# Kernel optimization log

Measured on AMD Instinct MI355X. Metric: run time of the kernel, lower is better.

The kernel has to match this reference:

```python
import jax, jax.numpy as jnp
import numpy as np

N = 100000      # nodes
E = 1600000     # edges (before self loops)
F_IN = 256      # num_features
HID = 8         # hid per head, layer 1
H1 = 8          # in_head
H2 = 4          # out_head
NCLS = 40       # num_classes


def setup_inputs() -> dict:
    key = jax.random.key(0)
    ks = jax.random.split(key, 10)
    p = lambda k, shape: jax.random.normal(k, shape, jnp.float32) * 0.1
    d1 = H1 * HID   # 64
    d2 = H2 * NCLS  # 160
    return dict(
        x=jax.random.normal(ks[0], (N, F_IN), jnp.float32),
        edge_index=jax.random.randint(ks[1], (2, E), 0, N),
        Wl1=p(ks[2], (F_IN, d1)), bl1=jnp.zeros((d1,), jnp.float32),
        Wr1=p(ks[3], (F_IN, d1)), br1=jnp.zeros((d1,), jnp.float32),
        att1=p(ks[4], (H1, HID)), b1=jnp.zeros((d1,), jnp.float32),
        Wl2=p(ks[5], (d1, d2)), bl2=jnp.zeros((d2,), jnp.float32),
        Wr2=p(ks[6], (d1, d2)), br2=jnp.zeros((d2,), jnp.float32),
        att2=p(ks[7], (H2, NCLS)), b2=jnp.zeros((NCLS,), jnp.float32),
    )


def gatv2_conv(x, src, dst, Wl, bl, Wr, br, att, bias, heads, ch, concat):
    """PyG GATv2Conv (eval mode): lin_l -> source/messages, lin_r -> target."""
    n = x.shape[0]
    xl = (x @ Wl + bl).reshape(n, heads, ch)   # source-side features
    xr = (x @ Wr + br).reshape(n, heads, ch)   # target-side features
    # edge-wise attention logits: LeakyReLU(x_i + x_j) . att
    e = jax.nn.leaky_relu(xl[src] + xr[dst], 0.2)          # [E, H, C]
    logits = jnp.einsum('ehc,hc->eh', e, att)               # [E, H]
    # segment softmax over incoming edges of each destination node
    m = jax.ops.segment_max(logits, dst, num_segments=n)    # [N, H]
    ex = jnp.exp(logits - m[dst])
    s = jax.ops.segment_sum(ex, dst, num_segments=n)        # [N, H]
    alpha = ex / (s[dst] + 1e-16)                           # [E, H]
    # scatter-add weighted source messages
    out = jax.ops.segment_sum(xl[src] * alpha[:, :, None], dst, num_segments=n)  # [N, H, C]
    if concat:
        return out.reshape(n, heads * ch) + bias
    return out.mean(axis=1) + bias


def reference(x, edge_index, Wl1, bl1, Wr1, br1, att1, b1,
              Wl2, bl2, Wr2, br2, att2, b2):
    n = x.shape[0]
    loop = jnp.arange(n)
    # PyG GATv2Conv default add_self_loops=True
    src = jnp.concatenate([edge_index[0], loop])
    dst = jnp.concatenate([edge_index[1], loop])
    # eval mode: all dropout (input, inter-layer, attention) disabled
    h = gatv2_conv(x, src, dst, Wl1, bl1, Wr1, br1, att1, b1, H1, HID, True)
    h = jax.nn.elu(h)
    out = gatv2_conv(h, src, dst, Wl2, bl2, Wr2, br2, att2, b2, H2, NCLS, False)
    return jax.nn.log_softmax(out, axis=1)
```

## Files before the change

### kernel.cpp

```cpp
#include <hip/hip_runtime.h>
#include <math.h>

#define NN 100000
#define EE 1600000
#define FIN 256
#define D1 64
#define D2 160
#define C2 40
#define PK1 264
#define PK2 72
#define NBUCK 391
#define CAP 5000

typedef unsigned short u16;
typedef __attribute__((ext_vector_type(8))) short bf16x8;
typedef __attribute__((ext_vector_type(4))) float f32x4;

__device__ __forceinline__ float bf2f(u16 u){ return __uint_as_float((unsigned)u << 16); }
__device__ __forceinline__ u16 f2bf(float f){
  unsigned b = __float_as_uint(f);
  return (u16)((b + 0x7FFFu + ((b >> 16) & 1u)) >> 16);
}

__global__ void wprep_k(const float* __restrict__ Wl1, const float* __restrict__ Wr1,
                        const float* __restrict__ att1,
                        const float* __restrict__ bl1, const float* __restrict__ br1,
                        const float* __restrict__ Wl2, const float* __restrict__ Wr2,
                        const float* __restrict__ att2,
                        const float* __restrict__ bl2, const float* __restrict__ br2,
                        float* __restrict__ WA1, float* __restrict__ BA1,
                        float* __restrict__ WA2, float* __restrict__ BA2){
  int t = threadIdx.x;
  {
    int k = t;
    #pragma unroll
    for (int j = 0; j < 16; ++j){
      const float* W = (j < 8) ? Wl1 : Wr1;
      int h = j & 7;
      float s = 0.f;
      #pragma unroll
      for (int c = 0; c < 8; ++c) s += W[(size_t)k*D1 + h*8 + c] * att1[h*8 + c];
      WA1[k*16 + j] = 0.6f * s;
    }
  }
  if (t < 64){
    int k = t;
    #pragma unroll
    for (int j = 0; j < 8; ++j){
      const float* W = (j < 4) ? Wl2 : Wr2;
      int h = j & 3;
      float s = 0.f;
      for (int c = 0; c < 40; ++c) s += W[(size_t)k*D2 + h*40 + c] * att2[h*40 + c];
      WA2[k*8 + j] = 0.6f * s;
    }
  }
  if (t >= 128 && t < 144){
    int j = t - 128;
    const float* B = (j < 8) ? bl1 : br1;
    int h = j & 7;
    float s = 0.f;
    #pragma unroll
    for (int c = 0; c < 8; ++c) s += B[h*8 + c] * att1[h*8 + c];
    BA1[j] = 0.6f * s;
  }
  if (t >= 160 && t < 168){
    int j = t - 160;
    const float* B = (j < 4) ? bl2 : br2;
    int h = j & 3;
    float s = 0.f;
    for (int c = 0; c < 40; ++c) s += B[h*40 + c] * att2[h*40 + c];
    BA2[j] = 0.6f * s;
  }
}

__global__ __launch_bounds__(256) void part1_k(const int* __restrict__ ei,
                                               int* __restrict__ bcnt,
                                               int* __restrict__ csrtmp){
  __shared__ int hist[NBUCK];
  __shared__ int gbase[NBUCK];
  int t = threadIdx.x;
  for (int i = t; i < NBUCK; i += 256) hist[i] = 0;
  __syncthreads();
  int rb[8], rr[8], rv[8];
  #pragma unroll
  for (int q = 0; q < 8; ++q){
    int e = blockIdx.x*2048 + q*256 + t;
    rb[q] = -1;
    if (e < EE){
      int s = ei[e], d = ei[EE + e];
      int b = d >> 8;
      rb[q] = b;
      rv[q] = s | ((d & 255) << 17);
      rr[q] = atomicAdd(&hist[b], 1);
    }
  }
  __syncthreads();
  for (int i = t; i < NBUCK; i += 256)
    if (hist[i] > 0) gbase[i] = atomicAdd(&bcnt[i], hist[i]);
  __syncthreads();
  #pragma unroll
  for (int q = 0; q < 8; ++q){
    if (rb[q] >= 0){
      int pos = gbase[rb[q]] + rr[q];
      if (pos < CAP) csrtmp[rb[q]*CAP + pos] = rv[q];
    }
  }
}

__global__ __launch_bounds__(256) void sort_k(const int* __restrict__ bcnt,
                                              const int* __restrict__ csrtmp,
                                              int* __restrict__ csr,
                                              int* __restrict__ off,
                                              int* __restrict__ end){
  __shared__ int cnt[256];
  __shared__ int sc[256];
  __shared__ int cur[256];
  int b = blockIdx.x, t = threadIdx.x;
  int E = bcnt[b]; if (E > CAP) E = CAP;
  cnt[t] = 0;
  __syncthreads();
  for (int i = t; i < E; i += 256){
    int v = csrtmp[b*CAP + i];
    atomicAdd(&cnt[(v >> 17) & 255], 1);
  }
  __syncthreads();
  int x = cnt[t];
  sc[t] = x;
  __syncthreads();
  for (int o = 1; o < 256; o <<= 1){
    int v = (t >= o) ? sc[t - o] : 0;
    __syncthreads();
    sc[t] += v;
    __syncthreads();
  }
  int excl = sc[t] - x;
  cur[t] = excl;
  int n = (b << 8) + t;
  if (n < NN){
    off[n] = b*CAP + excl;
    end[n] = b*CAP + excl + x;
  }
  __syncthreads();
  for (int i = t; i < E; i += 256){
    int v = csrtmp[b*CAP + i];
    int p = atomicAdd(&cur[(v >> 17) & 255], 1);
    csr[b*CAP + p] = v & 0x1FFFF;
  }
}

__global__ __launch_bounds__(256) void gemm1_mfma(
    const float* __restrict__ X,
    const float* __restrict__ Wl, const float* __restrict__ bl,
    const float* __restrict__ Wr, const float* __restrict__ br,
    const float* __restrict__ WA1, const float* __restrict__ BA1,
    u16* __restrict__ outl, u16* __restrict__ outr, float* __restrict__ ALR){
  __shared__ u16 WB[144*PK1];
  int t = threadIdx.x;
  #pragma unroll
  for (int q = 0; q < 16; ++q){
    int idx = t + 256*q;
    int k = idx >> 4, c4 = idx & 15;
    float4 vl = *reinterpret_cast<const float4*>(Wl + (size_t)k*D1 + c4*4);
    float4 vr = *reinterpret_cast<const float4*>(Wr + (size_t)k*D1 + c4*4);
    WB[(c4*4+0)*PK1 + k] = f2bf(vl.x); WB[(c4*4+1)*PK1 + k] = f2bf(vl.y);
    WB[(c4*4+2)*PK1 + k] = f2bf(vl.z); WB[(c4*4+3)*PK1 + k] = f2bf(vl.w);
    WB[(64+c4*4+0)*PK1 + k] = f2bf(vr.x); WB[(64+c4*4+1)*PK1 + k] = f2bf(vr.y);
    WB[(64+c4*4+2)*PK1 + k] = f2bf(vr.z); WB[(64+c4*4+3)*PK1 + k] = f2bf(vr.w);
  }
  #pragma unroll
  for (int q = 0; q < 16; ++q){
    int idx = t + 256*q;
    int k = idx >> 4, j = idx & 15;
    WB[(128+j)*PK1 + k] = f2bf(WA1[k*16 + j]);
  }
  __syncthreads();
  int w = t >> 6, l = t & 63;
  int g = l >> 4;
  int arow = blockIdx.x*64 + w*16 + (l & 15);
  if (arow >= NN) arow = NN-1;
  const float* xp = X + (size_t)arow*FIN + g*8;
  f32x4 acc[9] = {};
  #pragma unroll
  for (int kk = 0; kk < 8; ++kk){
    float4 a0 = *reinterpret_cast<const float4*>(xp + kk*32);
    float4 a1 = *reinterpret_cast<const float4*>(xp + kk*32 + 4);
    union { bf16x8 v; u16 u[8]; } A;
    A.u[0]=f2bf(a0.x); A.u[1]=f2bf(a0.y); A.u[2]=f2bf(a0.z); A.u[3]=f2bf(a0.w);
    A.u[4]=f2bf(a1.x); A.u[5]=f2bf(a1.y); A.u[6]=f2bf(a1.z); A.u[7]=f2bf(a1.w);
    const u16* wb = WB + (l & 15)*PK1 + kk*32 + g*8;
    #pragma unroll
    for (int c = 0; c < 9; ++c){
      bf16x8 B = *reinterpret_cast<const bf16x8*>(wb + c*16*PK1);
      acc[c] = __builtin_amdgcn_mfma_f32_16x16x32_bf16(A.v, B, acc[c], 0, 0, 0);
    }
  }
  int ocol = l & 15;
  int orow0 = blockIdx.x*64 + w*16 + g*4;
  #pragma unroll
  for (int c = 0; c < 8; ++c){
    bool left = (c < 4);
    int col = (left ? c : c-4)*16 + ocol;
    u16* op = left ? outl : outr;
    float bv = (left ? bl : br)[col];
    #pragma unroll
    for (int r = 0; r < 4; ++r){
      int row = orow0 + r;
      if (row < NN) op[(size_t)row*D1 + col] = f2bf(acc[c][r] + bv);
    }
  }
  {
    float bav = BA1[ocol];
    #pragma unroll
    for (int r = 0; r < 4; ++r){
      int row = orow0 + r;
      if (row < NN) ALR[(size_t)row*16 + ocol] = acc[8][r] + bav;
    }
  }
}

__global__ __launch_bounds__(256) void gemm2_mfma(
    const u16* __restrict__ H,
    const float* __restrict__ Wl, const float* __restrict__ bl,
    const float* __restrict__ Wr, const float* __restrict__ br,
    const float* __restrict__ WA2, const float* __restrict__ BA2,
    u16* __restrict__ outl, u16* __restrict__ outr, float* __restrict__ ALR){
  __shared__ u16 WB[336*PK2];
  int t = threadIdx.x;
  #pragma unroll
  for (int q = 0; q < 10; ++q){
    int idx = t + 256*q;
    int k = idx / 40, c4 = idx % 40;
    float4 vl = *reinterpret_cast<const float4*>(Wl + (size_t)k*D2 + c4*4);
    float4 vr = *reinterpret_cast<const float4*>(Wr + (size_t)k*D2 + c4*4);
    WB[(c4*4+0)*PK2 + k] = f2bf(vl.x); WB[(c4*4+1)*PK2 + k] = f2bf(vl.y);
    WB[(c4*4+2)*PK2 + k] = f2bf(vl.z); WB[(c4*4+3)*PK2 + k] = f2bf(vl.w);
    WB[(160+c4*4+0)*PK2 + k] = f2bf(vr.x); WB[(160+c4*4+1)*PK2 + k] = f2bf(vr.y);
    WB[(160+c4*4+2)*PK2 + k] = f2bf(vr.z); WB[(160+c4*4+3)*PK2 + k] = f2bf(vr.w);
  }
  #pragma unroll
  for (int q = 0; q < 2; ++q){
    int i2 = t + 256*q;
    int k = i2 >> 3, j = i2 & 7;
    WB[(320+j)*PK2 + k] = f2bf(WA2[k*8 + j]);
    WB[(328+j)*PK2 + k] = 0;
  }
  __syncthreads();
  int w = t >> 6, l = t & 63;
  int g = l >> 4;
  int arow = blockIdx.x*64 + w*16 + (l & 15);
  if (arow >= NN) arow = NN-1;
  const u16* hp = H + (size_t)arow*D1 + g*8;
  f32x4 acc[21] = {};
  #pragma unroll
  for (int kk = 0; kk < 2; ++kk){
    bf16x8 A = *reinterpret_cast<const bf16x8*>(hp + kk*32);
    const u16* wb = WB + (l & 15)*PK2 + kk*32 + g*8;
    #pragma unroll
    for (int c = 0; c < 21; ++c){
      bf16x8 B = *reinterpret_cast<const bf16x8*>(wb + c*16*PK2);
      acc[c] = __builtin_amdgcn_mfma_f32_16x16x32_bf16(A, B, acc[c], 0, 0, 0);
    }
  }
  int ocol = l & 15;
  int orow0 = blockIdx.x*64 + w*16 + g*4;
  #pragma unroll
  for (int c = 0; c < 20; ++c){
    bool left = (c < 10);
    int col = (left ? c : c-10)*16 + ocol;
    u16* op = left ? outl : outr;
    float bv = (left ? bl : br)[col];
    #pragma unroll
    for (int r = 0; r < 4; ++r){
      int row = orow0 + r;
      if (row < NN) op[(size_t)row*D2 + col] = f2bf(acc[c][r] + bv);
    }
  }
  if (ocol < 8){
    float bav = BA2[ocol];
    #pragma unroll
    for (int r = 0; r < 4; ++r){
      int row = orow0 + r;
      if (row < NN) ALR[(size_t)row*8 + ocol] = acc[20][r] + bav;
    }
  }
}

__global__ void l1_fused(const u16* __restrict__ xl, const u16* __restrict__ xr,
                         const int* __restrict__ off, const int* __restrict__ end,
                         const int* __restrict__ csr,
                         const float* __restrict__ att, const float* __restrict__ ALR,
                         const float* __restrict__ b, u16* __restrict__ out){
  int tid = threadIdx.x;
  int lane = tid & 63;
  int nh = lane >> 5, g = (lane >> 4) & 1, l = lane & 15;
  int n = blockIdx.x*8 + (tid >> 6)*2 + nh;
  if (n >= NN) return;
  int h = l >> 1;
  ushort4 xru = *reinterpret_cast<const ushort4*>(xr + (size_t)n*D1 + 4*l);
  float xrv[4] = {bf2f(xru.x), bf2f(xru.y), bf2f(xru.z), bf2f(xru.w)};
  float a04[4];
  #pragma unroll
  for (int k = 0; k < 4; ++k) a04[k] = 0.4f * att[4*l + k];
  float ARn = ALR[(size_t)n*16 + 8 + h];
  ushort4 xsu = *reinterpret_cast<const ushort4*>(xl + (size_t)n*D1 + 4*l);
  float xsv[4] = {bf2f(xsu.x), bf2f(xsu.y), bf2f(xsu.z), bf2f(xsu.w)};
  float ts = 0.f;
  #pragma unroll
  for (int k = 0; k < 4; ++k) ts += a04[k] * fabsf(xsv[k] + xrv[k]);
  ts += __shfl_xor(ts, 1);
  float ps = (g == 0) ? __expf(ts + ALR[(size_t)n*16 + h] + ARn) : 0.f;
  float s = ps, acc[4];
  #pragma unroll
  for (int k = 0; k < 4; ++k) acc[k] = ps * xsv[k];
  int p = off[n] + g, e1 = end[n];
  for (; p + 2 < e1; p += 4){
    int sa = csr[p], sb = csr[p+2];
    ushort4 ua = *reinterpret_cast<const ushort4*>(xl + (size_t)sa*D1 + 4*l);
    ushort4 ub = *reinterpret_cast<const ushort4*>(xl + (size_t)sb*D1 + 4*l);
    float ALa = ALR[(size_t)sa*16 + h], ALb = ALR[(size_t)sb*16 + h];
    float xa[4] = {bf2f(ua.x), bf2f(ua.y), bf2f(ua.z), bf2f(ua.w)};
    float xb[4] = {bf2f(ub.x), bf2f(ub.y), bf2f(ub.z), bf2f(ub.w)};
    float ta = 0.f, tb = 0.f;
    #pragma unroll
    for (int k = 0; k < 4; ++k){
      ta += a04[k] * fabsf(xa[k] + xrv[k]);
      tb += a04[k] * fabsf(xb[k] + xrv[k]);
    }
    ta += __shfl_xor(ta, 1);
    tb += __shfl_xor(tb, 1);
    float pa = __expf(ta + ALa + ARn);
    float pb = __expf(tb + ALb + ARn);
    s += pa + pb;
    #pragma unroll
    for (int k = 0; k < 4; ++k) acc[k] = fmaf(pa, xa[k], fmaf(pb, xb[k], acc[k]));
  }
  for (; p < e1; p += 2){
    int sa = csr[p];
    ushort4 ua = *reinterpret_cast<const ushort4*>(xl + (size_t)sa*D1 + 4*l);
    float ALa = ALR[(size_t)sa*16 + h];
    float xa[4] = {bf2f(ua.x), bf2f(ua.y), bf2f(ua.z), bf2f(ua.w)};
    float ta = 0.f;
    #pragma unroll
    for (int k = 0; k < 4; ++k) ta += a04[k] * fabsf(xa[k] + xrv[k]);
    ta += __shfl_xor(ta, 1);
    float pa = __expf(ta + ALa + ARn);
    s += pa;
    #pragma unroll
    for (int k = 0; k < 4; ++k) acc[k] = fmaf(pa, xa[k], acc[k]);
  }
  s += __shfl_xor(s, 16);
  #pragma unroll
  for (int k = 0; k < 4; ++k) acc[k] += __shfl_xor(acc[k], 16);
  if (g == 0){
    float inv = 1.f / (s + 1e-16f);
    ushort4 o;
    float v0 = acc[0]*inv + b[4*l+0]; o.x = f2bf(v0 > 0.f ? v0 : expm1f(v0));
    float v1 = acc[1]*inv + b[4*l+1]; o.y = f2bf(v1 > 0.f ? v1 : expm1f(v1));
    float v2 = acc[2]*inv + b[4*l+2]; o.z = f2bf(v2 > 0.f ? v2 : expm1f(v2));
    float v3 = acc[3]*inv + b[4*l+3]; o.w = f2bf(v3 > 0.f ? v3 : expm1f(v3));
    *reinterpret_cast<ushort4*>(out + (size_t)n*D1 + 4*l) = o;
  }
}

__global__ void l2_fused(const u16* __restrict__ xl, const u16* __restrict__ xr,
                         const int* __restrict__ off, const int* __restrict__ end,
                         const int* __restrict__ csr,
                         const float* __restrict__ att, const float* __restrict__ ALR,
                         const float* __restrict__ b, float* __restrict__ out){
  int tid = threadIdx.x;
  int lane = tid & 63;
  int nh = lane >> 5, g = (lane >> 4) & 1, l = lane & 15;
  int n = blockIdx.x*8 + (tid >> 6)*2 + nh;
  if (n >= NN) return;
  int h = l >> 2;
  int c0 = 10*l;
  float xrv[10], a04[10];
  #pragma unroll
  for (int k2 = 0; k2 < 5; ++k2){
    ushort2 u = *reinterpret_cast<const ushort2*>(xr + (size_t)n*D2 + c0 + 2*k2);
    xrv[2*k2] = bf2f(u.x); xrv[2*k2+1] = bf2f(u.y);
  }
  #pragma unroll
  for (int k = 0; k < 10; ++k) a04[k] = 0.4f * att[c0 + k];
  float ARn = ALR[(size_t)n*8 + 4 + h];
  float xsv[10];
  #pragma unroll
  for (int k2 = 0; k2 < 5; ++k2){
    ushort2 u = *reinterpret_cast<const ushort2*>(xl + (size_t)n*D2 + c0 + 2*k2);
    xsv[2*k2] = bf2f(u.x); xsv[2*k2+1] = bf2f(u.y);
  }
  float ts = 0.f;
  #pragma unroll
  for (int k = 0; k < 10; ++k) ts += a04[k] * fabsf(xsv[k] + xrv[k]);
  ts += __shfl_xor(ts, 1); ts += __shfl_xor(ts, 2);
  float ps = (g == 0) ? __expf(ts + ALR[(size_t)n*8 + h] + ARn) : 0.f;
  float s = ps, acc[10];
  #pragma unroll
  for (int k = 0; k < 10; ++k) acc[k] = ps * xsv[k];
  int p = off[n] + g, e1 = end[n];
  for (; p + 2 < e1; p += 4){
    int sa = csr[p], sb = csr[p+2];
    float ALa = ALR[(size_t)sa*8 + h], ALb = ALR[(size_t)sb*8 + h];
    float xa[10], xb[10];
    #pragma unroll
    for (int k2 = 0; k2 < 5; ++k2){
      ushort2 u = *reinterpret_cast<const ushort2*>(xl + (size_t)sa*D2 + c0 + 2*k2);
      xa[2*k2] = bf2f(u.x); xa[2*k2+1] = bf2f(u.y);
    }
    #pragma unroll
    for (int k2 = 0; k2 < 5; ++k2){
      ushort2 u = *reinterpret_cast<const ushort2*>(xl + (size_t)sb*D2 + c0 + 2*k2);
      xb[2*k2] = bf2f(u.x); xb[2*k2+1] = bf2f(u.y);
    }
    float ta = 0.f, tb = 0.f;
    #pragma unroll
    for (int k = 0; k < 10; ++k){
      ta += a04[k] * fabsf(xa[k] + xrv[k]);
      tb += a04[k] * fabsf(xb[k] + xrv[k]);
    }
    ta += __shfl_xor(ta, 1); ta += __shfl_xor(ta, 2);
    tb += __shfl_xor(tb, 1); tb += __shfl_xor(tb, 2);
    float pa = __expf(ta + ALa + ARn);
    float pb = __expf(tb + ALb + ARn);
    s += pa + pb;
    #pragma unroll
    for (int k = 0; k < 10; ++k) acc[k] = fmaf(pa, xa[k], fmaf(pb, xb[k], acc[k]));
  }
  for (; p < e1; p += 2){
    int sa = csr[p];
    float ALa = ALR[(size_t)sa*8 + h];
    float xa[10];
    #pragma unroll
    for (int k2 = 0; k2 < 5; ++k2){
      ushort2 u = *reinterpret_cast<const ushort2*>(xl + (size_t)sa*D2 + c0 + 2*k2);
      xa[2*k2] = bf2f(u.x); xa[2*k2+1] = bf2f(u.y);
    }
    float ta = 0.f;
    #pragma unroll
    for (int k = 0; k < 10; ++k) ta += a04[k] * fabsf(xa[k] + xrv[k]);
    ta += __shfl_xor(ta, 1); ta += __shfl_xor(ta, 2);
    float pa = __expf(ta + ALa + ARn);
    s += pa;
    #pragma unroll
    for (int k = 0; k < 10; ++k) acc[k] = fmaf(pa, xa[k], acc[k]);
  }
  s += __shfl_xor(s, 16);
  #pragma unroll
  for (int k = 0; k < 10; ++k) acc[k] += __shfl_xor(acc[k], 16);
  float inv = 1.f / (s + 1e-16f);
  float v[10];
  #pragma unroll
  for (int k = 0; k < 10; ++k){
    float o = acc[k] * inv;
    o += __shfl_xor(o, 4);
    o += __shfl_xor(o, 8);
    v[k] = o*0.25f + b[10*(l & 3) + k];
  }
  float mx = v[0];
  #pragma unroll
  for (int k = 1; k < 10; ++k) mx = fmaxf(mx, v[k]);
  mx = fmaxf(mx, __shfl_xor(mx, 1));
  mx = fmaxf(mx, __shfl_xor(mx, 2));
  float es = 0.f;
  #pragma unroll
  for (int k = 0; k < 10; ++k) es += __expf(v[k] - mx);
  es += __shfl_xor(es, 1);
  es += __shfl_xor(es, 2);
  float lse = mx + __logf(es);
  if (g == 0 && l < 4){
    float* op = out + (size_t)n*C2 + 10*l;
    #pragma unroll
    for (int k2 = 0; k2 < 5; ++k2)
      *reinterpret_cast<float2*>(op + 2*k2) = make_float2(v[2*k2] - lse, v[2*k2+1] - lse);
  }
}

extern "C" void kernel_launch(void* const* d_in, const int* in_sizes, int n_in,
                              void* d_out, int out_size, void* d_ws, size_t ws_size,
                              hipStream_t stream){
  const float* x    = (const float*)d_in[0];
  const int*   ei   = (const int*)  d_in[1];
  const float* Wl1  = (const float*)d_in[2];
  const float* bl1  = (const float*)d_in[3];
  const float* Wr1  = (const float*)d_in[4];
  const float* br1  = (const float*)d_in[5];
  const float* att1 = (const float*)d_in[6];
  const float* b1   = (const float*)d_in[7];
  const float* Wl2  = (const float*)d_in[8];
  const float* bl2  = (const float*)d_in[9];
  const float* Wr2  = (const float*)d_in[10];
  const float* br2  = (const float*)d_in[11];
  const float* att2 = (const float*)d_in[12];
  const float* b2   = (const float*)d_in[13];
  float* out = (float*)d_out;

  char* ws = (char*)d_ws;
  u16*   B1     = (u16*)  (ws);
  u16*   B2     = (u16*)  (ws + 13000000);
  u16*   h1     = (u16*)  (ws + 26000000);
  u16*   B3     = (u16*)  (ws + 39000000);
  u16*   B4     = (u16*)  (ws + 71000000);
  int*   csrtmp = (int*)  (ws + 71000000);
  float* ALR1   = (float*)(ws + 103000000);
  float* ALR2   = (float*)(ws + 110000000);
  float* WA1    = (float*)(ws + 113300000);
  float* BA1    = (float*)(ws + 113330000);
  float* WA2    = (float*)(ws + 113340000);
  float* BA2    = (float*)(ws + 113350000);
  int*   off    = (int*)  (ws + 113400000);
  int*   end    = (int*)  (ws + 113900000);
  int*   bcnt   = (int*)  (ws + 114400000);
  int*   csr    = (int*)  (ws + 114500000);
  const int blk = 256;
  const int MB = (NN + 63)/64;

  hipMemsetAsync(bcnt, 0, (size_t)NBUCK*4, stream);
  part1_k<<<(EE + 2047)/2048, blk, 0, stream>>>(ei, bcnt, csrtmp);
  sort_k <<<NBUCK, blk, 0, stream>>>(bcnt, csrtmp, csr, off, end);
  wprep_k<<<1, blk, 0, stream>>>(Wl1, Wr1, att1, bl1, br1,
                                 Wl2, Wr2, att2, bl2, br2, WA1, BA1, WA2, BA2);

  gemm1_mfma<<<MB, blk, 0, stream>>>(x, Wl1, bl1, Wr1, br1, WA1, BA1, B1, B2, ALR1);
  l1_fused  <<<(NN + 7)/8, blk, 0, stream>>>(B1, B2, off, end, csr, att1, ALR1, b1, h1);

  gemm2_mfma<<<MB, blk, 0, stream>>>(h1, Wl2, bl2, Wr2, br2, WA2, BA2, B3, B4, ALR2);
  l2_fused  <<<(NN + 7)/8, blk, 0, stream>>>(B3, B4, off, end, csr, att2, ALR2, b2, out);
}
```

Before: 381.3 us.

## Fold target attention term out and store exp source weight inline with features

The target-side linear attention term is constant per destination, so it cancels in the softmax and is dropped. The source-side term is precomputed as exp() in bf16 and stored in padded columns of the source feature rows, replacing a separate fp32 ALR gather per edge. The row strides are padded (72/168) so the per-edge weight arrives with the feature fetch, and wprep is parallelised across 19 blocks. This costs bf16 precision on the exp weight and removes the max-free logit offset, so it risks overflow or loss of accuracy.

```diff
diff --git a/kernel.cpp b/kernel.cpp
--- a/kernel.cpp
+++ b/kernel.cpp
@@ -7,6 +7,8 @@
 #define D1 64
 #define D2 160
 #define C2 40
+#define P1R 72
+#define P2R 168
 #define PK1 264
 #define PK2 72
 #define NBUCK 391
@@ -30,45 +32,39 @@
                         const float* __restrict__ bl2, const float* __restrict__ br2,
                         float* __restrict__ WA1, float* __restrict__ BA1,
                         float* __restrict__ WA2, float* __restrict__ BA2){
-  int t = threadIdx.x;
-  {
-    int k = t;
-    #pragma unroll
-    for (int j = 0; j < 16; ++j){
-      const float* W = (j < 8) ? Wl1 : Wr1;
-      int h = j & 7;
+  int t = blockIdx.x*256 + threadIdx.x;
+  if (t < 4096){
+    int k = t >> 4, j = t & 15;
+    float v = 0.f;
+    if (j < 8){
       float s = 0.f;
       #pragma unroll
-      for (int c = 0; c < 8; ++c) s += W[(size_t)k*D1 + h*8 + c] * att1[h*8 + c];
-      WA1[k*16 + j] = 0.6f * s;
-    }
-  }
-  if (t < 64){
-    int k = t;
-    #pragma unroll
-    for (int j = 0; j < 8; ++j){
-      const float* W = (j < 4) ? Wl2 : Wr2;
-      int h = j & 3;
+      for (int c = 0; c < 8; ++c) s += Wl1[(size_t)k*D1 + j*8 + c] * att1[j*8 + c];
+      v = 0.6f * s;
+    }
+    WA1[t] = v;
+  } else if (t < 4608){
+    int i = t - 4096;
+    int k = i >> 3, j = i & 7;
+    float v = 0.f;
+    if (j < 4){
       float s = 0.f;
-      for (int c = 0; c < 40; ++c) s += W[(size_t)k*D2 + h*40 + c] * att2[h*40 + c];
-      WA2[k*8 + j] = 0.6f * s;
-    }
-  }
-  if (t >= 128 && t < 144){
-    int j = t - 128;
-    const float* B = (j < 8) ? bl1 : br1;
-    int h = j & 7;
+      #pragma unroll
+      for (int c = 0; c < 40; ++c) s += Wl2[(size_t)k*D2 + j*40 + c] * att2[j*40 + c];
+      v = 0.6f * s;
+    }
+    WA2[i] = v;
+  } else if (t < 4616){
+    int j = t - 4608;
     float s = 0.f;
     #pragma unroll
-    for (int c = 0; c < 8; ++c) s += B[h*8 + c] * att1[h*8 + c];
+    for (int c = 0; c < 8; ++c) s += bl1[j*8 + c] * att1[j*8 + c];
     BA1[j] = 0.6f * s;
-  }
-  if (t >= 160 && t < 168){
-    int j = t - 160;
-    const float* B = (j < 4) ? bl2 : br2;
-    int h = j & 3;
+  } else if (t < 4620){
+    int j = t - 4616;
     float s = 0.f;
-    for (int c = 0; c < 40; ++c) s += B[h*40 + c] * att2[h*40 + c];
+    #pragma unroll
+    for (int c = 0; c < 40; ++c) s += bl2[j*40 + c] * att2[j*40 + c];
     BA2[j] = 0.6f * s;
   }
 }
@@ -153,7 +149,7 @@
     const float* __restrict__ Wl, const float* __restrict__ bl,
     const float* __restrict__ Wr, const float* __restrict__ br,
     const float* __restrict__ WA1, const float* __restrict__ BA1,
-    u16* __restrict__ outl, u16* __restrict__ outr, float* __restrict__ ALR){
+    u16* __restrict__ outl, u16* __restrict__ outr){
   __shared__ u16 WB[144*PK1];
   int t = threadIdx.x;
   #pragma unroll
@@ -205,15 +201,15 @@
     #pragma unroll
     for (int r = 0; r < 4; ++r){
       int row = orow0 + r;
-      if (row < NN) op[(size_t)row*D1 + col] = f2bf(acc[c][r] + bv);
-    }
-  }
-  {
+      if (row < NN) op[(size_t)row*P1R + col] = f2bf(acc[c][r] + bv);
+    }
+  }
+  if (ocol < 8){
     float bav = BA1[ocol];
     #pragma unroll
     for (int r = 0; r < 4; ++r){
       int row = orow0 + r;
-      if (row < NN) ALR[(size_t)row*16 + ocol] = acc[8][r] + bav;
+      if (row < NN) outl[(size_t)row*P1R + 64 + ocol] = f2bf(__expf(acc[8][r] + bav));
     }
   }
 }
@@ -223,7 +219,7 @@
     const float* __restrict__ Wl, const float* __restrict__ bl,
     const float* __restrict__ Wr, const float* __restrict__ br,
     const float* __restrict__ WA2, const float* __restrict__ BA2,
-    u16* __restrict__ outl, u16* __restrict__ outr, float* __restrict__ ALR){
+    u16* __restrict__ outl, u16* __restrict__ outr){
   __shared__ u16 WB[336*PK2];
   int t = threadIdx.x;
   #pragma unroll
@@ -272,15 +268,15 @@
     #pragma unroll
     for (int r = 0; r < 4; ++r){
       int row = orow0 + r;
-      if (row < NN) op[(size_t)row*D2 + col] = f2bf(acc[c][r] + bv);
-    }
-  }
-  if (ocol < 8){
+      if (row < NN) op[(size_t)row*P2R + col] = f2bf(acc[c][r] + bv);
+    }
+  }
+  if (ocol < 4){
     float bav = BA2[ocol];
     #pragma unroll
     for (int r = 0; r < 4; ++r){
       int row = orow0 + r;
-      if (row < NN) ALR[(size_t)row*8 + ocol] = acc[20][r] + bav;
+      if (row < NN) outl[(size_t)row*P2R + 160 + ocol] = f2bf(__expf(acc[20][r] + bav));
     }
   }
 }
@@ -288,7 +284,7 @@
 __global__ void l1_fused(const u16* __restrict__ xl, const u16* __restrict__ xr,
                          const int* __restrict__ off, const int* __restrict__ end,
                          const int* __restrict__ csr,
-                         const float* __restrict__ att, const float* __restrict__ ALR,
+                         const float* __restrict__ att,
                          const float* __restrict__ b, u16* __restrict__ out){
   int tid = threadIdx.x;
   int lane = tid & 63;
@@ -296,54 +292,55 @@
   int n = blockIdx.x*8 + (tid >> 6)*2 + nh;
   if (n >= NN) return;
   int h = l >> 1;
-  ushort4 xru = *reinterpret_cast<const ushort4*>(xr + (size_t)n*D1 + 4*l);
+  ushort4 xru = *reinterpret_cast<const ushort4*>(xr + (size_t)n*P1R + 4*l);
   float xrv[4] = {bf2f(xru.x), bf2f(xru.y), bf2f(xru.z), bf2f(xru.w)};
   float a04[4];
   #pragma unroll
   for (int k = 0; k < 4; ++k) a04[k] = 0.4f * att[4*l + k];
-  float ARn = ALR[(size_t)n*16 + 8 + h];
-  ushort4 xsu = *reinterpret_cast<const ushort4*>(xl + (size_t)n*D1 + 4*l);
+  ushort4 xsu = *reinterpret_cast<const ushort4*>(xl + (size_t)n*P1R + 4*l);
+  float wN = bf2f(xl[(size_t)n*P1R + 64 + h]);
   float xsv[4] = {bf2f(xsu.x), bf2f(xsu.y), bf2f(xsu.z), bf2f(xsu.w)};
   float ts = 0.f;
   #pragma unroll
-  for (int k = 0; k < 4; ++k) ts += a04[k] * fabsf(xsv[k] + xrv[k]);
+  for (int k = 0; k < 4; ++k) ts = fmaf(a04[k], fabsf(xsv[k] + xrv[k]), ts);
   ts += __shfl_xor(ts, 1);
-  float ps = (g == 0) ? __expf(ts + ALR[(size_t)n*16 + h] + ARn) : 0.f;
+  float ps = (g == 0) ? __expf(ts) * wN : 0.f;
   float s = ps, acc[4];
   #pragma unroll
   for (int k = 0; k < 4; ++k) acc[k] = ps * xsv[k];
   int p = off[n] + g, e1 = end[n];
   for (; p + 2 < e1; p += 4){
     int sa = csr[p], sb = csr[p+2];
-    ushort4 ua = *reinterpret_cast<const ushort4*>(xl + (size_t)sa*D1 + 4*l);
-    ushort4 ub = *reinterpret_cast<const ushort4*>(xl + (size_t)sb*D1 + 4*l);
-    float ALa = ALR[(size_t)sa*16 + h], ALb = ALR[(size_t)sb*16 + h];
+    ushort4 ua = *reinterpret_cast<const ushort4*>(xl + (size_t)sa*P1R + 4*l);
+    ushort4 ub = *reinterpret_cast<const ushort4*>(xl + (size_t)sb*P1R + 4*l);
+    float wA = bf2f(xl[(size_t)sa*P1R + 64 + h]);
+    float wB = bf2f(xl[(size_t)sb*P1R + 64 + h]);
     float xa[4] = {bf2f(ua.x), bf2f(ua.y), bf2f(ua.z), bf2f(ua.w)};
     float xb[4] = {bf2f(ub.x), bf2f(ub.y), bf2f(ub.z), bf2f(ub.w)};
     float ta = 0.f, tb = 0.f;
     #pragma unroll
     for (int k = 0; k < 4; ++k){
-      ta += a04[k] * fabsf(xa[k] + xrv[k]);
-      tb += a04[k] * fabsf(xb[k] + xrv[k]);
+      ta = fmaf(a04[k], fabsf(xa[k] + xrv[k]), ta);
+      tb = fmaf(a04[k], fabsf(xb[k] + xrv[k]), tb);
     }
     ta += __shfl_xor(ta, 1);
     tb += __shfl_xor(tb, 1);
-    float pa = __expf(ta + ALa + ARn);
-    float pb = __expf(tb + ALb + ARn);
+    float pa = __expf(ta) * wA;
+    float pb = __expf(tb) * wB;
     s += pa + pb;
     #pragma unroll
     for (int k = 0; k < 4; ++k) acc[k] = fmaf(pa, xa[k], fmaf(pb, xb[k], acc[k]));
   }
   for (; p < e1; p += 2){
     int sa = csr[p];
-    ushort4 ua = *reinterpret_cast<const ushort4*>(xl + (size_t)sa*D1 + 4*l);
-    float ALa = ALR[(size_t)sa*16 + h];
+    ushort4 ua = *reinterpret_cast<const ushort4*>(xl + (size_t)sa*P1R + 4*l);
+    float wA = bf2f(xl[(size_t)sa*P1R + 64 + h]);
     float xa[4] = {bf2f(ua.x), bf2f(ua.y), bf2f(ua.z), bf2f(ua.w)};
     float ta = 0.f;
     #pragma unroll
-    for (int k = 0; k < 4; ++k) ta += a04[k] * fabsf(xa[k] + xrv[k]);
+    for (int k = 0; k < 4; ++k) ta = fmaf(a04[k], fabsf(xa[k] + xrv[k]), ta);
     ta += __shfl_xor(ta, 1);
-    float pa = __expf(ta + ALa + ARn);
+    float pa = __expf(ta) * wA;
     s += pa;
     #pragma unroll
     for (int k = 0; k < 4; ++k) acc[k] = fmaf(pa, xa[k], acc[k]);
@@ -365,7 +362,7 @@
 __global__ void l2_fused(const u16* __restrict__ xl, const u16* __restrict__ xr,
                          const int* __restrict__ off, const int* __restrict__ end,
                          const int* __restrict__ csr,
-                         const float* __restrict__ att, const float* __restrict__ ALR,
+                         const float* __restrict__ att,
                          const float* __restrict__ b, float* __restrict__ out){
   int tid = threadIdx.x;
   int lane = tid & 63;
@@ -377,69 +374,76 @@
   float xrv[10], a04[10];
   #pragma unroll
   for (int k2 = 0; k2 < 5; ++k2){
-    ushort2 u = *reinterpret_cast<const ushort2*>(xr + (size_t)n*D2 + c0 + 2*k2);
+    ushort2 u = *reinterpret_cast<const ushort2*>(xr + (size_t)n*P2R + c0 + 2*k2);
     xrv[2*k2] = bf2f(u.x); xrv[2*k2+1] = bf2f(u.y);
   }
   #pragma unroll
   for (int k = 0; k < 10; ++k) a04[k] = 0.4f * att[c0 + k];
-  float ARn = ALR[(size_t)n*8 + 4 + h];
   float xsv[10];
   #pragma unroll
   for (int k2 = 0; k2 < 5; ++k2){
-    ushort2 u = *reinterpret_cast<const ushort2*>(xl + (size_t)n*D2 + c0 + 2*k2);
+    ushort2 u = *reinterpret_cast<const ushort2*>(xl + (size_t)n*P2R + c0 + 2*k2);
     xsv[2*k2] = bf2f(u.x); xsv[2*k2+1] = bf2f(u.y);
   }
+  float wN = bf2f(xl[(size_t)n*P2R + 160 + h]);
   float ts = 0.f;
   #pragma unroll
-  for (int k = 0; k < 10; ++k) ts += a04[k] * fabsf(xsv[k] + xrv[k]);
+  for (int k = 0; k < 10; ++k) ts = fmaf(a04[k], fabsf(xsv[k] + xrv[k]), ts);
   ts += __shfl_xor(ts, 1); ts += __shfl_xor(ts, 2);
-  float ps = (g == 0) ? __expf(ts + ALR[(size_t)n*8 + h] + ARn) : 0.f;
+  float ps = (g == 0) ? __expf(ts) * wN : 0.f;
   float s = ps, acc[10];
   #pragma unroll
   for (int k = 0; k < 10; ++k) acc[k] = ps * xsv[k];
   int p = off[n] + g, e1 = end[n];
   for (; p + 2 < e1; p += 4){
     int sa = csr[p], sb = csr[p+2];
-    float ALa = ALR[(size_t)sa*8 + h], ALb = ALR[(size_t)sb*8 + h];
+    const u16* ra = xl + (size_t)sa*P2R + c0;
+    const u16* rb = xl + (size_t)sb*P2R + c0;
+    int dwa[5], dwb[5];
+    #pragma unroll
+    for (int d = 0; d < 5; ++d) dwa[d] = *reinterpret_cast<const int*>(ra + 2*d);
+    #pragma unroll
+    for (int d = 0; d < 5; ++d) dwb[d] = *reinterpret_cast<const int*>(rb + 2*d);
+    float wA = bf2f(xl[(size_t)sa*P2R + 160 + h]);
+    float wB = bf2f(xl[(size_t)sb*P2R + 160 + h]);
     float xa[10], xb[10];
     #pragma unroll
-    for (int k2 = 0; k2 < 5; ++k2){
-      ushort2 u = *reinterpret_cast<const ushort2*>(xl + (size_t)sa*D2 + c0 + 2*k2);
-      xa[2*k2] = bf2f(u.x); xa[2*k2+1] = bf2f(u.y);
-    }
-    #pragma unroll
-    for (int k2 = 0; k2 < 5; ++k2){
-      ushort2 u = *reinterpret_cast<const ushort2*>(xl + (size_t)sb*D2 + c0 + 2*k2);
-      xb[2*k2] = bf2f(u.x); xb[2*k2+1] = bf2f(u.y);
+    for (int d = 0; d < 5; ++d){
+      xa[2*d]   = __uint_as_float(((unsigned)dwa[d]) << 16);
+      xa[2*d+1] = __uint_as_float(((unsigned)dwa[d]) & 0xFFFF0000u);
+      xb[2*d]   = __uint_as_float(((unsigned)dwb[d]) << 16);
+      xb[2*d+1] = __uint_as_float(((unsigned)dwb[d]) & 0xFFFF0000u);
     }
     float ta = 0.f, tb = 0.f;
     #pragma unroll
     for (int k = 0; k < 10; ++k){
-      ta += a04[k] * fabsf(xa[k] + xrv[k]);
-      tb += a04[k] * fabsf(xb[k] + xrv[k]);
+      ta = fmaf(a04[k], fabsf(xa[k] + xrv[k]), ta);
+      tb = fmaf(a04[k], fabsf(xb[k] + xrv[k]), tb);
     }
     ta += __shfl_xor(ta, 1); ta += __shfl_xor(ta, 2);
     tb += __shfl_xor(tb, 1); tb += __shfl_xor(tb, 2);
-    float pa = __expf(ta + ALa + ARn);
-    float pb = __expf(tb + ALb + ARn);
+    float pa = __expf(ta) * wA;
+    float pb = __expf(tb) * wB;
     s += pa + pb;
     #pragma unroll
     for (int k = 0; k < 10; ++k) acc[k] = fmaf(pa, xa[k], fmaf(pb, xb[k], acc[k]));
   }
   for (; p < e1; p += 2){
     int sa = csr[p];
-    float ALa = ALR[(size_t)sa*8 + h];
+    const u16* rp = xl + (size_t)sa*P2R + c0;
+    float wA = bf2f(xl[(size_t)sa*P2R + 160 + h]);
     float xa[10];
     #pragma unroll
-    for (int k2 = 0; k2 < 5; ++k2){
-      ushort2 u = *reinterpret_cast<const ushort2*>(xl + (size_t)sa*D2 + c0 + 2*k2);
-      xa[2*k2] = bf2f(u.x); xa[2*k2+1] = bf2f(u.y);
+    for (int d = 0; d < 5; ++d){
+      int u = *reinterpret_cast<const int*>(rp + 2*d);
+      xa[2*d]   = __uint_as_float(((unsigned)u) << 16);
+      xa[2*d+1] = __uint_as_float(((unsigned)u) & 0xFFFF0000u);
     }
     float ta = 0.f;
     #pragma unroll
-    for (int k = 0; k < 10; ++k) ta += a04[k] * fabsf(xa[k] + xrv[k]);
+    for (int k = 0; k < 10; ++k) ta = fmaf(a04[k], fabsf(xa[k] + xrv[k]), ta);
     ta += __shfl_xor(ta, 1); ta += __shfl_xor(ta, 2);
-    float pa = __expf(ta + ALa + ARn);
+    float pa = __expf(ta) * wA;
     s += pa;
     #pragma unroll
     for (int k = 0; k < 10; ++k) acc[k] = fmaf(pa, xa[k], acc[k]);
@@ -496,33 +500,31 @@
 
   char* ws = (char*)d_ws;
   u16*   B1     = (u16*)  (ws);
-  u16*   B2     = (u16*)  (ws + 13000000);
-  u16*   h1     = (u16*)  (ws + 26000000);
-  u16*   B3     = (u16*)  (ws + 39000000);
-  u16*   B4     = (u16*)  (ws + 71000000);
-  int*   csrtmp = (int*)  (ws + 71000000);
-  float* ALR1   = (float*)(ws + 103000000);
-  float* ALR2   = (float*)(ws + 110000000);
-  float* WA1    = (float*)(ws + 113300000);
-  float* BA1    = (float*)(ws + 113330000);
-  float* WA2    = (float*)(ws + 113340000);
-  float* BA2    = (float*)(ws + 113350000);
-  int*   off    = (int*)  (ws + 113400000);
-  int*   end    = (int*)  (ws + 113900000);
-  int*   bcnt   = (int*)  (ws + 114400000);
-  int*   csr    = (int*)  (ws + 114500000);
+  u16*   B2     = (u16*)  (ws + 15000000);
+  u16*   h1     = (u16*)  (ws + 30000000);
+  u16*   B3     = (u16*)  (ws + 43000000);
+  u16*   B4     = (u16*)  (ws + 77000000);
+  int*   csrtmp = (int*)  (ws + 77000000);
+  float* WA1    = (float*)(ws + 111000000);
+  float* BA1    = (float*)(ws + 111100000);
+  float* WA2    = (float*)(ws + 111200000);
+  float* BA2    = (float*)(ws + 111300000);
+  int*   off    = (int*)  (ws + 111400000);
+  int*   end    = (int*)  (ws + 111900000);
+  int*   bcnt   = (int*)  (ws + 112400000);
+  int*   csr    = (int*)  (ws + 112500000);
   const int blk = 256;
   const int MB = (NN + 63)/64;
 
   hipMemsetAsync(bcnt, 0, (size_t)NBUCK*4, stream);
   part1_k<<<(EE + 2047)/2048, blk, 0, stream>>>(ei, bcnt, csrtmp);
   sort_k <<<NBUCK, blk, 0, stream>>>(bcnt, csrtmp, csr, off, end);
-  wprep_k<<<1, blk, 0, stream>>>(Wl1, Wr1, att1, bl1, br1,
-                                 Wl2, Wr2, att2, bl2, br2, WA1, BA1, WA2, BA2);
-
-  gemm1_mfma<<<MB, blk, 0, stream>>>(x, Wl1, bl1, Wr1, br1, WA1, BA1, B1, B2, ALR1);
-  l1_fused  <<<(NN + 7)/8, blk, 0, stream>>>(B1, B2, off, end, csr, att1, ALR1, b1, h1);
-
-  gemm2_mfma<<<MB, blk, 0, stream>>>(h1, Wl2, bl2, Wr2, br2, WA2, BA2, B3, B4, ALR2);
-  l2_fused  <<<(NN + 7)/8, blk, 0, stream>>>(B3, B4, off, end, csr, att2, ALR2, b2, out);
-}
+  wprep_k<<<19, blk, 0, stream>>>(Wl1, Wr1, att1, bl1, br1,
+                                  Wl2, Wr2, att2, bl2, br2, WA1, BA1, WA2, BA2);
+
+  gemm1_mfma<<<MB, blk, 0, stream>>>(x, Wl1, bl1, Wr1, br1, WA1, BA1, B1, B2);
+  l1_fused  <<<(NN + 7)/8, blk, 0, stream>>>(B1, B2, off, end, csr, att1, b1, h1);
+
+  gemm2_mfma<<<MB, blk, 0, stream>>>(h1, Wl2, bl2, Wr2, br2, WA2, BA2, B3, B4);
+  l2_fused  <<<(NN + 7)/8, blk, 0, stream>>>(B3, B4, off, end, csr, att2, b2, out);
+}
```

New measurement: 350.0 us. -8.2%, faster.
